# Optimization experiments

Hardware: AMD Instinct MI355X
Metric: run time of the kernel (lower is better)

Reference implementation:

```python
import jax, jax.numpy as jnp
import numpy as np

EMBED_DIM = 1024
B, C, H, W = 32, 1024, 32, 32


def _conv1x1(x, w, b):
    # x: [B,C,H,W], w: [O,C] (squeezed 1x1 conv kernel), b: [O]
    return jnp.einsum('bchw,oc->bohw', x, w) + b[None, :, None, None]


def setup_inputs() -> dict:
    key = jax.random.key(0)
    ks = jax.random.split(key, 12)
    s = 1.0 / np.sqrt(C)  # torch Conv2d default init scale (uniform bound)
    inp = {
        'shape_map': jax.random.normal(ks[0], (B, C, H, W), jnp.float32),
        'img_map': jax.random.normal(ks[1], (B, C, H, W), jnp.float32),
        'wq': jax.random.uniform(ks[2], (C, C), jnp.float32, -s, s),
        'bq': jax.random.uniform(ks[3], (C,), jnp.float32, -s, s),
        'wk': jax.random.uniform(ks[4], (C, C), jnp.float32, -s, s),
        'bk': jax.random.uniform(ks[5], (C,), jnp.float32, -s, s),
        'wv': jax.random.uniform(ks[6], (C, C), jnp.float32, -s, s),
        'bv': jax.random.uniform(ks[7], (C,), jnp.float32, -s, s),
        'wc': jax.random.uniform(ks[8], (C, C), jnp.float32, -s, s),
        'bc': jax.random.uniform(ks[9], (C,), jnp.float32, -s, s),
    }
    return inp


def reference(shape_map, img_map, wq, bq, wk, bk, wv, bv, wc, bc):
    # QKV embeddings: 1x1 conv + tanh (dropout is identity at inference)
    q = jnp.tanh(_conv1x1(shape_map, wq, bq))  # [B,C,H,W]
    k = jnp.tanh(_conv1x1(img_map, wk, bk))
    v = jnp.tanh(_conv1x1(img_map, wv, bv))

    hw = H * W
    q_flat = q.reshape(B, C, hw)
    k_flat = k.reshape(B, C, hw)
    v_flat = v.reshape(B, C, hw)

    # channel-attention: scores over channel pairs, contracted over spatial HW
    scores = jnp.einsum('bcs,bds->bcd', q_flat, k_flat) / jnp.sqrt(
        jnp.asarray(C, q_flat.dtype))  # [B,C,C]
    weights = jax.nn.softmax(scores, axis=-1)
    new_v = jnp.einsum('bcd,bds->bcs', weights, v_flat).reshape(B, C, H, W)

    out = _conv1x1(new_v, wc, bc) + shape_map
    return out
```

## Files before the change

kernel.cpp:

```cpp
#include <hip/hip_runtime.h>


typedef __bf16 bf16x8 __attribute__((ext_vector_type(8)));
typedef float floatx4 __attribute__((ext_vector_type(4)));

__device__ __forceinline__ unsigned short f2bf(float f) {
  union { float f; unsigned int u; } c; c.f = f;
  unsigned int u = c.u;
  u += 0x7fffu + ((u >> 16) & 1u);
  return (unsigned short)(u >> 16);
}

__device__ __forceinline__ float tanh_fast(float x) {
  x = fminf(15.0f, fmaxf(-15.0f, x));
  float t = __expf(2.0f * x);
  return (t - 1.0f) / (t + 1.0f);
}

__device__ __forceinline__ void gemm_core(
    const unsigned short* __restrict__ Ab,
    const unsigned short* __restrict__ Bb,
    int m0, int n0,
    unsigned short* lA, unsigned short* lB,
    floatx4 acc[4][4])
{
  constexpr int K = 1024;
  const int tid  = threadIdx.x;
  const int w    = tid >> 6;
  const int lane = tid & 63;
  const int quad = lane >> 4;
  const int lm   = lane & 15;
  const int wm   = (w >> 1) * 64;
  const int wn   = (w & 1) * 64;
  const int xr   = lm & 7;

  const int srow = lane >> 3;
  const int sg   = (lane & 7) ^ srow;
  const unsigned short* gA0 = Ab + (size_t)(m0 + srow) * K + sg * 8;
  const unsigned short* gB0 = Bb + (size_t)(n0 + srow) * K + sg * 8;

  for (int k0 = 0; k0 < K; k0 += 64) {
#pragma unroll
    for (int i = 0; i < 4; ++i) {
      const int q = w * 4 + i;
      __builtin_amdgcn_global_load_lds(
          (__attribute__((address_space(1))) void*)(gA0 + (size_t)q * 8 * K + k0),
          (__attribute__((address_space(3))) void*)(lA + q * 512), 16, 0, 0);
      __builtin_amdgcn_global_load_lds(
          (__attribute__((address_space(1))) void*)(gB0 + (size_t)q * 8 * K + k0),
          (__attribute__((address_space(3))) void*)(lB + q * 512), 16, 0, 0);
    }
    __syncthreads();

#pragma unroll
    for (int ks = 0; ks < 2; ++ks) {
      bf16x8 af[4], bfv[4];
#pragma unroll
      for (int i = 0; i < 4; ++i) {
        const int row = wm + 16 * i + lm;
        af[i] = *(const bf16x8*)(lA + row * 64 + (((ks * 4 + quad) ^ xr) * 8));
      }
#pragma unroll
      for (int j = 0; j < 4; ++j) {
        const int row = wn + 16 * j + lm;
        bfv[j] = *(const bf16x8*)(lB + row * 64 + (((ks * 4 + quad) ^ xr) * 8));
      }
#pragma unroll
      for (int i = 0; i < 4; ++i)
#pragma unroll
        for (int j = 0; j < 4; ++j)
          acc[i][j] = __builtin_amdgcn_mfma_f32_16x16x32_bf16(
              af[i], bfv[j], acc[i][j], 0, 0, 0);
    }
    __syncthreads();
  }
}

template<int OUT_F32, int BIAS_MODE , int TANH_ON, int RESID_ON>
__global__ __launch_bounds__(256, 2)
void gemm_bt(const unsigned short* __restrict__ A,
             const unsigned short* __restrict__ B,
             void* __restrict__ Cv,
             const float* __restrict__ bias,
             const float* __restrict__ resid,
             float scale,
             size_t sA, size_t sB, size_t sC, size_t sR)
{
  __shared__ unsigned short lA[128 * 64];
  __shared__ unsigned short lB[128 * 64];
  const int m0 = blockIdx.y * 128, n0 = blockIdx.x * 128;
  const int lane = threadIdx.x & 63, w = threadIdx.x >> 6;
  const int quad = lane >> 4, lm = lane & 15;
  const int wm = (w >> 1) * 64, wn = (w & 1) * 64;

  floatx4 acc[4][4];
#pragma unroll
  for (int i = 0; i < 4; ++i)
#pragma unroll
    for (int j = 0; j < 4; ++j) acc[i][j] = (floatx4)(0.0f);

  gemm_core(A + blockIdx.z * sA, B + blockIdx.z * sB, m0, n0, lA, lB, acc);

  float* Cf = (float*)Cv + blockIdx.z * sC;
  unsigned short* Cb = (unsigned short*)Cv + blockIdx.z * sC;
  const float* rp = RESID_ON ? (resid + blockIdx.z * sR) : (const float*)0;

#pragma unroll
  for (int i = 0; i < 4; ++i) {
    const int mbase = m0 + wm + 16 * i + quad * 4;
#pragma unroll
    for (int j = 0; j < 4; ++j) {
      const int n = n0 + wn + 16 * j + lm;
#pragma unroll
      for (int r = 0; r < 4; ++r) {
        const int m = mbase + r;
        float val = acc[i][j][r] * scale;
        if (BIAS_MODE == 1) val += bias[m];
        if (BIAS_MODE == 2) val += bias[n];
        if (TANH_ON) val = tanh_fast(val);
        if (RESID_ON) val += rp[(size_t)m * 1024 + n];
        if (OUT_F32) Cf[(size_t)m * 1024 + n] = val;
        else         Cb[(size_t)m * 1024 + n] = f2bf(val);
      }
    }
  }
}

__global__ __launch_bounds__(256, 2)
void qkv_gemm(const unsigned short* __restrict__ wqb,
              const unsigned short* __restrict__ wkb,
              const unsigned short* __restrict__ wvb,
              const unsigned short* __restrict__ Xt,
              const unsigned short* __restrict__ Yt,
              unsigned short* __restrict__ Qb,
              unsigned short* __restrict__ Kb,
              unsigned short* __restrict__ Vt,
              const float* __restrict__ bq,
              const float* __restrict__ bk,
              const float* __restrict__ bv,
              size_t sBf, int nb)
{
  __shared__ unsigned short lA[128 * 64];
  __shared__ unsigned short lB[128 * 64];
  const int z = blockIdx.z;
  int op, b;
  if (z >= 2 * nb)      { op = 2; b = z - 2 * nb; }
  else if (z >= nb)     { op = 1; b = z - nb; }
  else                  { op = 0; b = z; }

  const unsigned short *A, *B;
  unsigned short* C;
  const float* bias;
  int biasM;
  if (op == 0)      { A = wqb;            B = Xt + b * sBf; C = Qb + b * sBf; bias = bq; biasM = 1; }
  else if (op == 1) { A = wkb;            B = Yt + b * sBf; C = Kb + b * sBf; bias = bk; biasM = 1; }
  else              { A = Yt + b * sBf;   B = wvb;          C = Vt + b * sBf; bias = bv; biasM = 0; }

  const int m0 = blockIdx.y * 128, n0 = blockIdx.x * 128;
  const int lane = threadIdx.x & 63, w = threadIdx.x >> 6;
  const int quad = lane >> 4, lm = lane & 15;
  const int wm = (w >> 1) * 64, wn = (w & 1) * 64;

  floatx4 acc[4][4];
#pragma unroll
  for (int i = 0; i < 4; ++i)
#pragma unroll
    for (int j = 0; j < 4; ++j) acc[i][j] = (floatx4)(0.0f);

  gemm_core(A, B, m0, n0, lA, lB, acc);

#pragma unroll
  for (int i = 0; i < 4; ++i) {
    const int mbase = m0 + wm + 16 * i + quad * 4;
#pragma unroll
    for (int j = 0; j < 4; ++j) {
      const int n = n0 + wn + 16 * j + lm;
      const float bn = biasM ? 0.0f : bias[n];
#pragma unroll
      for (int r = 0; r < 4; ++r) {
        const int m = mbase + r;
        float val = acc[i][j][r] + (biasM ? bias[m] : bn);
        val = tanh_fast(val);
        C[(size_t)m * 1024 + n] = f2bf(val);
      }
    }
  }
}

__global__ __launch_bounds__(256)
void transpose2(const float* __restrict__ in0, const float* __restrict__ in1,
                unsigned short* __restrict__ out0, unsigned short* __restrict__ out1,
                size_t sIn, size_t sOut, int nb)
{
  __shared__ float tile[32][33];
  const int z = blockIdx.z;
  const float* in;
  unsigned short* out;
  if (z < nb) { in = in0 + (size_t)z * sIn;        out = out0 + (size_t)z * sOut; }
  else        { in = in1 + (size_t)(z - nb) * sIn; out = out1 + (size_t)(z - nb) * sOut; }

  const int x  = blockIdx.x * 32 + threadIdx.x;
  const int y0 = blockIdx.y * 32;
#pragma unroll
  for (int k = 0; k < 32; k += 8)
    tile[threadIdx.y + k][threadIdx.x] =
        in[(size_t)(y0 + threadIdx.y + k) * 1024 + x];
  __syncthreads();
  const int xo  = blockIdx.y * 32 + threadIdx.x;
  const int yo0 = blockIdx.x * 32;
#pragma unroll
  for (int k = 0; k < 32; k += 8)
    out[(size_t)(yo0 + threadIdx.y + k) * 1024 + xo] =
        f2bf(tile[threadIdx.x][threadIdx.y + k]);
}

__global__ __launch_bounds__(256)
void softmax_rows(const float* __restrict__ S, unsigned short* __restrict__ W,
                  size_t sS, size_t sW)
{
  const float* s = S + blockIdx.y * sS + (size_t)blockIdx.x * 1024;
  unsigned short* w = W + blockIdx.y * sW + (size_t)blockIdx.x * 1024;
  const int t = threadIdx.x;
  float4 v = ((const float4*)s)[t];
  float mx = fmaxf(fmaxf(v.x, v.y), fmaxf(v.z, v.w));
#pragma unroll
  for (int off = 32; off > 0; off >>= 1)
    mx = fmaxf(mx, __shfl_xor(mx, off));
  __shared__ float redm[4], reds[4];
  const int lane = t & 63, wv = t >> 6;
  if (lane == 0) redm[wv] = mx;
  __syncthreads();
  mx = fmaxf(fmaxf(redm[0], redm[1]), fmaxf(redm[2], redm[3]));
  float e0 = __expf(v.x - mx), e1 = __expf(v.y - mx),
        e2 = __expf(v.z - mx), e3 = __expf(v.w - mx);
  float sum = e0 + e1 + e2 + e3;
#pragma unroll
  for (int off = 32; off > 0; off >>= 1)
    sum += __shfl_xor(sum, off);
  if (lane == 0) reds[wv] = sum;
  __syncthreads();
  sum = reds[0] + reds[1] + reds[2] + reds[3];
  const float inv = 1.0f / sum;
  w[4 * t + 0] = f2bf(e0 * inv);
  w[4 * t + 1] = f2bf(e1 * inv);
  w[4 * t + 2] = f2bf(e2 * inv);
  w[4 * t + 3] = f2bf(e3 * inv);
}

__global__ __launch_bounds__(256)
void cvt_all(const float* __restrict__ s0, const float* __restrict__ s1,
             const float* __restrict__ s2, const float* __restrict__ s3,
             unsigned short* __restrict__ d0, unsigned short* __restrict__ d1,
             unsigned short* __restrict__ d2, unsigned short* __restrict__ d3)
{
  const float* in; unsigned short* out;
  switch (blockIdx.y) {
    case 0: in = s0; out = d0; break;
    case 1: in = s1; out = d1; break;
    case 2: in = s2; out = d2; break;
    default: in = s3; out = d3; break;
  }
  const int i = blockIdx.x * 256 + threadIdx.x;
  float4 v = ((const float4*)in)[i];
  ushort4 o;
  o.x = f2bf(v.x); o.y = f2bf(v.y); o.z = f2bf(v.z); o.w = f2bf(v.w);
  ((ushort4*)out)[i] = o;
}

extern "C" void kernel_launch(void* const* d_in, const int* in_sizes, int n_in,
                              void* d_out, int out_size, void* d_ws, size_t ws_size,
                              hipStream_t stream)
{
  const float* shape_map = (const float*)d_in[0];
  const float* img_map   = (const float*)d_in[1];
  const float* wq = (const float*)d_in[2];
  const float* bq = (const float*)d_in[3];
  const float* wk = (const float*)d_in[4];
  const float* bk = (const float*)d_in[5];
  const float* wv = (const float*)d_in[6];
  const float* bv = (const float*)d_in[7];
  const float* wc = (const float*)d_in[8];
  const float* bc = (const float*)d_in[9];
  float* out = (float*)d_out;

  const size_t ELT = 1024 * 1024;
  const size_t MB  = 1024 * 1024;
  char* ws = (char*)d_ws;

  unsigned short* wq_b = (unsigned short*)(ws + 0 * 2 * MB);
  unsigned short* wk_b = (unsigned short*)(ws + 1 * 2 * MB);
  unsigned short* wv_b = (unsigned short*)(ws + 2 * 2 * MB);
  unsigned short* wc_b = (unsigned short*)(ws + 3 * 2 * MB);
  char* slots = ws + 8 * MB;
  const size_t slotBytes = 10 * MB;
  int nslots = (ws_size > 8 * MB + slotBytes)
                   ? (int)((ws_size - 8 * MB) / slotBytes) : 1;
  if (nslots > 32) nslots = 32;
  if (nslots < 1)  nslots = 1;

  cvt_all<<<dim3(1024, 4), 256, 0, stream>>>(wq, wk, wv, wc,
                                             wq_b, wk_b, wv_b, wc_b);

  const size_t sBf = slotBytes / 2;
  const size_t sF  = slotBytes / 4;

  for (int c0 = 0; c0 < 32; c0 += nslots) {
    const int nb = (32 - c0 < nslots) ? (32 - c0) : nslots;

    unsigned short* Xt  = (unsigned short*)(slots + 0);
    unsigned short* Yt  = (unsigned short*)(slots + 2 * MB);
    float*          Sm  = (float*)(slots + 0);
    unsigned short* Qb  = (unsigned short*)(slots + 4 * MB);
    unsigned short* Kb  = (unsigned short*)(slots + 6 * MB);
    unsigned short* Vt  = (unsigned short*)(slots + 8 * MB);
    unsigned short* Wsm = Qb;
    unsigned short* NVt = Kb;

    transpose2<<<dim3(32, 32, 2 * nb), dim3(32, 8), 0, stream>>>(
        shape_map + (size_t)c0 * ELT, img_map + (size_t)c0 * ELT,
        Xt, Yt, ELT, sBf, nb);

    qkv_gemm<<<dim3(8, 8, 3 * nb), 256, 0, stream>>>(
        wq_b, wk_b, wv_b, Xt, Yt, Qb, Kb, Vt, bq, bk, bv, sBf, nb);

    gemm_bt<1, 0, 0, 0><<<dim3(8, 8, nb), 256, 0, stream>>>(
        Qb, Kb, Sm, nullptr, nullptr, 0.03125f, sBf, sBf, sF, 0);

    softmax_rows<<<dim3(1024, nb), 256, 0, stream>>>(Sm, Wsm, sF, sBf);

    gemm_bt<0, 0, 0, 0><<<dim3(8, 8, nb), 256, 0, stream>>>(
        Vt, Wsm, NVt, nullptr, nullptr, 1.0f, sBf, sBf, sBf, 0);

    gemm_bt<1, 1, 0, 1><<<dim3(8, 8, nb), 256, 0, stream>>>(
        wc_b, NVt, out + (size_t)c0 * ELT, bc,
        shape_map + (size_t)c0 * ELT, 1.0f, 0, sBf, ELT, ELT);
  }
}
```

Baseline: 1.011 ms.

## Double-buffer LDS tiles with K=32 steps to overlap global loads with MFMA

Restructures the shared GEMM core from single-buffered 64-wide K tiles, which had two barriers per step, into double-buffered 32-wide K tiles with one barrier per step. The next tile's global-to-LDS load is issued before computing on the current one, so memory latency can overlap with MFMA work. The swizzle is adjusted to the narrower 32-element rows. It also simplifies tanh by dropping the clamp and using a 1-2/(t+1) form, which handles overflow to infinity correctly. The trade-off is twice as many barrier iterations with less MFMA work between them, with LDS size unchanged.

```diff
diff --git a/kernel.cpp b/kernel.cpp
--- a/kernel.cpp
+++ b/kernel.cpp
@@ -3,6 +3,9 @@
 
 typedef __bf16 bf16x8 __attribute__((ext_vector_type(8)));
 typedef float floatx4 __attribute__((ext_vector_type(4)));
+
+#define AS1(p) ((__attribute__((address_space(1))) void*)(p))
+#define AS3(p) ((__attribute__((address_space(3))) void*)(p))
 
 __device__ __forceinline__ unsigned short f2bf(float f) {
   union { float f; unsigned int u; } c; c.f = f;
@@ -12,16 +15,15 @@
 }
 
 __device__ __forceinline__ float tanh_fast(float x) {
-  x = fminf(15.0f, fmaxf(-15.0f, x));
   float t = __expf(2.0f * x);
-  return (t - 1.0f) / (t + 1.0f);
+  return 1.0f - 2.0f / (t + 1.0f);
 }
 
 __device__ __forceinline__ void gemm_core(
     const unsigned short* __restrict__ Ab,
     const unsigned short* __restrict__ Bb,
     int m0, int n0,
-    unsigned short* lA, unsigned short* lB,
+    unsigned short* lds,
     floatx4 acc[4][4])
 {
   constexpr int K = 1024;
@@ -32,47 +34,59 @@
   const int lm   = lane & 15;
   const int wm   = (w >> 1) * 64;
   const int wn   = (w & 1) * 64;
-  const int xr   = lm & 7;
-
-  const int srow = lane >> 3;
-  const int sg   = (lane & 7) ^ srow;
-  const unsigned short* gA0 = Ab + (size_t)(m0 + srow) * K + sg * 8;
-  const unsigned short* gB0 = Bb + (size_t)(n0 + srow) * K + sg * 8;
-
-  for (int k0 = 0; k0 < K; k0 += 64) {
+  const int xr   = lm & 3;
+
+  const int srow = lane >> 2;
+  const int sg   = (lane & 3) ^ (srow & 3);
+  const int q0   = w * 2;
+
+  const unsigned short* gA0 = Ab + (size_t)(m0 + q0 * 16 + srow) * K + sg * 8;
+  const unsigned short* gA1 = gA0 + (size_t)16 * K;
+  const unsigned short* gB0 = Bb + (size_t)(n0 + q0 * 16 + srow) * K + sg * 8;
+  const unsigned short* gB1 = gB0 + (size_t)16 * K;
+
+  unsigned short* dA0 = lds + q0 * 512;
+  unsigned short* dB0 = lds + 4096 + q0 * 512;
+
+  __builtin_amdgcn_global_load_lds(AS1(gA0), AS3(dA0),        16, 0, 0);
+  __builtin_amdgcn_global_load_lds(AS1(gA1), AS3(dA0 + 512),  16, 0, 0);
+  __builtin_amdgcn_global_load_lds(AS1(gB0), AS3(dB0),        16, 0, 0);
+  __builtin_amdgcn_global_load_lds(AS1(gB1), AS3(dB0 + 512),  16, 0, 0);
+
+  for (int k0 = 0; k0 < 32; ++k0) {
+    __syncthreads();
+
+    if (k0 + 1 < 32) {
+      const int kk = (k0 + 1) * 32;
+      unsigned short* da = lds + ((k0 + 1) & 1) * 8192 + q0 * 512;
+      unsigned short* db = da + 4096;
+      __builtin_amdgcn_global_load_lds(AS1(gA0 + kk), AS3(da),       16, 0, 0);
+      __builtin_amdgcn_global_load_lds(AS1(gA1 + kk), AS3(da + 512), 16, 0, 0);
+      __builtin_amdgcn_global_load_lds(AS1(gB0 + kk), AS3(db),       16, 0, 0);
+      __builtin_amdgcn_global_load_lds(AS1(gB1 + kk), AS3(db + 512), 16, 0, 0);
+    }
+
+    const unsigned short* la = lds + (k0 & 1) * 8192;
+    const unsigned short* lb = la + 4096;
+
+    bf16x8 af[4], bfv[4];
 #pragma unroll
     for (int i = 0; i < 4; ++i) {
-      const int q = w * 4 + i;
-      __builtin_amdgcn_global_load_lds(
-          (__attribute__((address_space(1))) void*)(gA0 + (size_t)q * 8 * K + k0),
-          (__attribute__((address_space(3))) void*)(lA + q * 512), 16, 0, 0);
-      __builtin_amdgcn_global_load_lds(
-          (__attribute__((address_space(1))) void*)(gB0 + (size_t)q * 8 * K + k0),
-          (__attribute__((address_space(3))) void*)(lB + q * 512), 16, 0, 0);
-    }
-    __syncthreads();
-
-#pragma unroll
-    for (int ks = 0; ks < 2; ++ks) {
-      bf16x8 af[4], bfv[4];
-#pragma unroll
-      for (int i = 0; i < 4; ++i) {
-        const int row = wm + 16 * i + lm;
-        af[i] = *(const bf16x8*)(lA + row * 64 + (((ks * 4 + quad) ^ xr) * 8));
-      }
-#pragma unroll
-      for (int j = 0; j < 4; ++j) {
-        const int row = wn + 16 * j + lm;
-        bfv[j] = *(const bf16x8*)(lB + row * 64 + (((ks * 4 + quad) ^ xr) * 8));
-      }
-#pragma unroll
-      for (int i = 0; i < 4; ++i)
-#pragma unroll
-        for (int j = 0; j < 4; ++j)
-          acc[i][j] = __builtin_amdgcn_mfma_f32_16x16x32_bf16(
-              af[i], bfv[j], acc[i][j], 0, 0, 0);
-    }
-    __syncthreads();
+      const int row = wm + 16 * i + lm;
+      af[i] = *(const bf16x8*)(la + row * 32 + ((quad ^ xr) * 8));
+    }
+#pragma unroll
+    for (int j = 0; j < 4; ++j) {
+      const int row = wn + 16 * j + lm;
+      bfv[j] = *(const bf16x8*)(lb + row * 32 + ((quad ^ xr) * 8));
+    }
+
+#pragma unroll
+    for (int i = 0; i < 4; ++i)
+#pragma unroll
+      for (int j = 0; j < 4; ++j)
+        acc[i][j] = __builtin_amdgcn_mfma_f32_16x16x32_bf16(
+            af[i], bfv[j], acc[i][j], 0, 0, 0);
   }
 }
 
@@ -86,8 +100,7 @@
              float scale,
              size_t sA, size_t sB, size_t sC, size_t sR)
 {
-  __shared__ unsigned short lA[128 * 64];
-  __shared__ unsigned short lB[128 * 64];
+  __shared__ unsigned short lds[16384];
   const int m0 = blockIdx.y * 128, n0 = blockIdx.x * 128;
   const int lane = threadIdx.x & 63, w = threadIdx.x >> 6;
   const int quad = lane >> 4, lm = lane & 15;
@@ -99,7 +112,7 @@
 #pragma unroll
     for (int j = 0; j < 4; ++j) acc[i][j] = (floatx4)(0.0f);
 
-  gemm_core(A + blockIdx.z * sA, B + blockIdx.z * sB, m0, n0, lA, lB, acc);
+  gemm_core(A + blockIdx.z * sA, B + blockIdx.z * sB, m0, n0, lds, acc);
 
   float* Cf = (float*)Cv + blockIdx.z * sC;
   unsigned short* Cb = (unsigned short*)Cv + blockIdx.z * sC;
@@ -140,8 +153,7 @@
               const float* __restrict__ bv,
               size_t sBf, int nb)
 {
-  __shared__ unsigned short lA[128 * 64];
-  __shared__ unsigned short lB[128 * 64];
+  __shared__ unsigned short lds[16384];
   const int z = blockIdx.z;
   int op, b;
   if (z >= 2 * nb)      { op = 2; b = z - 2 * nb; }
@@ -152,9 +164,9 @@
   unsigned short* C;
   const float* bias;
   int biasM;
-  if (op == 0)      { A = wqb;            B = Xt + b * sBf; C = Qb + b * sBf; bias = bq; biasM = 1; }
-  else if (op == 1) { A = wkb;            B = Yt + b * sBf; C = Kb + b * sBf; bias = bk; biasM = 1; }
-  else              { A = Yt + b * sBf;   B = wvb;          C = Vt + b * sBf; bias = bv; biasM = 0; }
+  if (op == 0)      { A = wqb;          B = Xt + b * sBf; C = Qb + b * sBf; bias = bq; biasM = 1; }
+  else if (op == 1) { A = wkb;          B = Yt + b * sBf; C = Kb + b * sBf; bias = bk; biasM = 1; }
+  else              { A = Yt + b * sBf; B = wvb;          C = Vt + b * sBf; bias = bv; biasM = 0; }
 
   const int m0 = blockIdx.y * 128, n0 = blockIdx.x * 128;
   const int lane = threadIdx.x & 63, w = threadIdx.x >> 6;
@@ -167,7 +179,7 @@
 #pragma unroll
     for (int j = 0; j < 4; ++j) acc[i][j] = (floatx4)(0.0f);
 
-  gemm_core(A, B, m0, n0, lA, lB, acc);
+  gemm_core(A, B, m0, n0, lds, acc);
 
 #pragma unroll
   for (int i = 0; i < 4; ++i) {
```

Result: slower. 1.041 ms (+2.9%).
